# Optimization experiments

Hardware: AMD Instinct MI355X
Metric: run time of the kernel (lower is better)

## Reference

```python
import jax, jax.numpy as jnp
import numpy as np

N = 50000
E = 1_600_000
IN_C = 128
OUT_C = 128


def _glorot(key, shape):
    fan_in, fan_out = shape[0], shape[1]
    s = jnp.sqrt(6.0 / (fan_in + fan_out))
    return jax.random.uniform(key, shape, jnp.float32, -s, s)


def setup_inputs() -> dict:
    key = jax.random.key(0)
    ks = jax.random.split(key, 32)
    inp = {
        'X': jax.random.normal(ks[0], (N, IN_C), jnp.float32),
        'edge_index': jax.random.randint(ks[1], (2, E), 0, N, jnp.int64),
        'edge_weight': jax.random.uniform(ks[2], (E,), jnp.float32),
        'H': jax.random.normal(ks[3], (N, OUT_C), jnp.float32),
        'C': jax.random.normal(ks[4], (N, OUT_C), jnp.float32),
    }
    i = 5
    for g in ('i', 'f', 'c', 'o'):
        inp[f'Wx_{g}'] = _glorot(ks[i], (IN_C, OUT_C)); i += 1
        inp[f'bx_{g}'] = jnp.zeros((OUT_C,), jnp.float32)
        inp[f'Wh_{g}'] = _glorot(ks[i], (OUT_C, OUT_C)); i += 1
        inp[f'bh_{g}'] = jnp.zeros((OUT_C,), jnp.float32)
    for g in ('i', 'f', 'o'):
        inp[f'w_c_{g}'] = _glorot(ks[i], (1, OUT_C)); i += 1
    for g in ('i', 'f', 'c', 'o'):
        inp[f'b_{g}'] = jnp.zeros((1, OUT_C), jnp.float32)
    return inp


def reference(X, edge_index, edge_weight, H, C,
              Wx_i, bx_i, Wh_i, bh_i,
              Wx_f, bx_f, Wh_f, bh_f,
              Wx_c, bx_c, Wh_c, bh_c,
              Wx_o, bx_o, Wh_o, bh_o,
              w_c_i, w_c_f, w_c_o,
              b_i, b_f, b_c, b_o):
    n = X.shape[0]
    src, dst = edge_index[0], edge_index[1]
    # GCN normalization (add_self_loops=False): deg from destination (in-degree)
    deg = jax.ops.segment_sum(edge_weight, dst, num_segments=n)
    dis = jnp.where(deg > 0, jax.lax.rsqrt(jnp.where(deg > 0, deg, 1.0)), 0.0)
    norm = dis[src] * edge_weight * dis[dst]  # [E]

    def gcn(x, W, b):
        xw = x @ W                       # [n, OUT_C]
        msg = xw[src] * norm[:, None]    # gather + scale, [E, OUT_C]
        return jax.ops.segment_sum(msg, dst, num_segments=n) + b

    I = jax.nn.sigmoid(gcn(X, Wx_i, bx_i) + gcn(H, Wh_i, bh_i) + w_c_i * C + b_i)
    Fg = jax.nn.sigmoid(gcn(X, Wx_f, bx_f) + gcn(H, Wh_f, bh_f) + w_c_f * C + b_f)
    T = jnp.tanh(gcn(X, Wx_c, bx_c) + gcn(H, Wh_c, bh_c) + b_c)
    Cn = Fg * C + I * T
    O = jax.nn.sigmoid(gcn(X, Wx_o, bx_o) + gcn(H, Wh_o, bh_o) + w_c_o * Cn + b_o)
    Hn = O * jnp.tanh(Cn)
    return Hn, Cn
```

## Files before the change

### kernel.cpp

```cpp
#include <hip/hip_runtime.h>

__device__ __forceinline__ float bf2f(unsigned short u){
    union { unsigned int i; float f; } v; v.i = ((unsigned int)u) << 16; return v.f;
}
__device__ __forceinline__ unsigned short f2bf(float f){
    union { unsigned int i; float f; } v; v.f = f;
    unsigned int i = v.i;
    unsigned int r = i + 0x7FFFu + ((i >> 16) & 1u);
    return (unsigned short)(r >> 16);
}
__device__ __forceinline__ float sigm(float x){ return 1.0f / (1.0f + __expf(-x)); }

__device__ __forceinline__ float ldsel(const void* p, size_t idx, int fF){
    float r;
    if (fF) r = ((const float*)p)[idx];
    else    r = bf2f(((const unsigned short*)p)[idx]);
    return r;
}

typedef __attribute__((ext_vector_type(8))) short s8v;
typedef __attribute__((ext_vector_type(4))) float f4v;

__global__ void k_detect(const unsigned short* __restrict__ X,
                         const int* __restrict__ ei, int* __restrict__ flags){
    __shared__ int cnt, nz;
    if (threadIdx.x == 0){ cnt = 0; nz = 0; }
    __syncthreads();
    int ok = 0;
    for (int i = threadIdx.x; i < 2048; i += 256){
        int e = (X[i] >> 7) & 0xFF;
        if (e >= 96 && e <= 160) ok++;
    }
    atomicAdd(&cnt, ok);
    int nzl = 0;
    for (int i = threadIdx.x; i < 128; i += 256)
        if (ei[2*i + 1] != 0) nzl++;
    atomicAdd(&nz, nzl);
    __syncthreads();
    if (threadIdx.x == 0){
        flags[0] = (cnt < 1843) ? 1 : 0;
        flags[1] = (nz == 0)   ? 1 : 0;
    }
}

struct PackArgs {
    const void* Wx[4];
    const void* Wh[4];
    const void* bx[4];
    const void* bh[4];
};

__global__ void k_fused1(const void* __restrict__ X, const void* __restrict__ H,
                         unsigned int* __restrict__ XHb32,
                         const int* __restrict__ ei, int* __restrict__ cnt,
                         int* __restrict__ off,
                         PackArgs pa, unsigned short* __restrict__ Bp,
                         float* __restrict__ bias,
                         const int* __restrict__ flags,
                         int nbT, int nbC, int E, int N){
    int b = blockIdx.x;
    int fF = flags[0];
    if (b < nbT){
        int t = b*256 + threadIdx.x;
        if (t >= N * 64) return;
        int n = t >> 6, l = t & 63;
        unsigned int xw, hw;
        if (fF){
            float2 xv = ((const float2*)X)[(size_t)n*64 + l];
            float2 hv = ((const float2*)H)[(size_t)n*64 + l];
            xw = ((unsigned int)f2bf(xv.y) << 16) | f2bf(xv.x);
            hw = ((unsigned int)f2bf(hv.y) << 16) | f2bf(hv.x);
        } else {
            xw = ((const unsigned int*)X)[(size_t)n*64 + l];
            hw = ((const unsigned int*)H)[(size_t)n*64 + l];
        }
        XHb32[(size_t)n*128 + l]      = xw;
        XHb32[(size_t)n*128 + 64 + l] = hw;
    } else if (b < nbT + nbC){
        int e = (b - nbT)*256 + threadIdx.x;
        if (e >= E) return;
        int fI = flags[1];
        int d = fI ? ei[2*(size_t)E + 2*(size_t)e] : ei[(size_t)E + e];
        if ((unsigned)d >= (unsigned)N) return;
        off[e] = atomicAdd(&cnt[d], 1);
    } else {
        int t = (b - nbT - nbC)*256 + threadIdx.x;
        if (t < 4*8*8*64*8){
            int j    =  t        & 7;
            int lane = (t >> 3)  & 63;
            int kb   = (t >> 9)  & 7;
            int ct   = (t >> 12) & 7;
            int g    = (t >> 15) & 3;
            int k   = kb*32 + (lane >> 4)*8 + j;
            int col = ct*16 + (lane & 15);
            const void* p; size_t idx;
            if (k < 128){ p = pa.Wx[g]; idx = (size_t)k*128 + col; }
            else        { p = pa.Wh[g]; idx = (size_t)(k-128)*128 + col; }
            unsigned short v;
            if (fF) v = f2bf(((const float*)p)[idx]);
            else    v = ((const unsigned short*)p)[idx];
            Bp[t] = v;
        }
        if (t < 512){
            int g = t >> 7, c = t & 127;
            bias[t] = ldsel(pa.bx[g], c, fF) + ldsel(pa.bh[g], c, fF);
        }
    }
}

__global__ void k_scanA(const int* __restrict__ cnt, int* __restrict__ bsum, int n){
    __shared__ int sh[256];
    int t = threadIdx.x, i = blockIdx.x * 256 + t;
    sh[t] = (i < n) ? cnt[i] : 0;
    __syncthreads();
    for (int o = 128; o > 0; o >>= 1){
        if (t < o) sh[t] += sh[t + o];
        __syncthreads();
    }
    if (t == 0) bsum[blockIdx.x] = sh[0];
}
__global__ void k_scanB(const int* __restrict__ bsum, int* __restrict__ bsumoff, int nb){
    __shared__ int sh[256];
    int t = threadIdx.x;
    int v = (t < nb) ? bsum[t] : 0;
    sh[t] = v;
    __syncthreads();
    for (int o = 1; o < 256; o <<= 1){
        int u = (t >= o) ? sh[t - o] : 0;
        __syncthreads();
        sh[t] += u;
        __syncthreads();
    }
    bsumoff[t] = sh[t] - v;
}
__global__ void k_scanC(const int* __restrict__ cnt, const int* __restrict__ bsumoff,
                        int* __restrict__ rowstart, int n){
    __shared__ int sh[256];
    int t = threadIdx.x, i = blockIdx.x * 256 + t;
    int v = (i < n) ? cnt[i] : 0;
    sh[t] = v;
    __syncthreads();
    for (int o = 1; o < 256; o <<= 1){
        int u = (t >= o) ? sh[t - o] : 0;
        __syncthreads();
        sh[t] += u;
        __syncthreads();
    }
    int incl = sh[t];
    if (i < n)     rowstart[i] = bsumoff[blockIdx.x] + incl - v;
    if (i == n-1)  rowstart[n] = bsumoff[blockIdx.x] + incl;
}

__global__ void k_scatter(const int* __restrict__ ei, const void* __restrict__ ew,
                          const int* __restrict__ rowstart, const int* __restrict__ off,
                          int2* __restrict__ recs, const int* __restrict__ flags,
                          int E, int N){
    int e = blockIdx.x * 256 + threadIdx.x;
    if (e >= E) return;
    int fF = flags[0], fI = flags[1];
    int s, d;
    if (fI){ s = ei[2*(size_t)e]; d = ei[2*(size_t)E + 2*(size_t)e]; }
    else   { s = ei[e];           d = ei[(size_t)E + e]; }
    if ((unsigned)d >= (unsigned)N) return;
    float w = 0.f; int ss = 0;
    if ((unsigned)s < (unsigned)N){ w = ldsel(ew, e, fF); ss = s; }
    int2 r; r.x = ss; r.y = __float_as_int(w);
    recs[rowstart[d] + off[e]] = r;
}

__global__ __launch_bounds__(256)
void k_degdis(const int2* __restrict__ recs, const int* __restrict__ rowstart,
              float* __restrict__ dis, int N){
    int gw = (blockIdx.x * 256 + threadIdx.x) >> 6;
    int lane = threadIdx.x & 63;
    if (gw >= N) return;
    int beg = rowstart[gw], end = rowstart[gw + 1];
    float sw = 0.f;
    for (int i = beg + lane; i < end; i += 64) sw += __int_as_float(recs[i].y);
    for (int o = 32; o > 0; o >>= 1) sw += __shfl_down(sw, o);
    if (lane == 0) dis[gw] = (sw > 0.f) ? rsqrtf(sw) : 0.f;
}

__global__ __launch_bounds__(256)
void k_gather(const int2* __restrict__ recs, const int* __restrict__ rowstart,
              const float* __restrict__ dis, const unsigned int* __restrict__ XHb32,
              unsigned int* __restrict__ AXH32, int N){
    int gw = (blockIdx.x * 256 + threadIdx.x) >> 6;
    int lane = threadIdx.x & 63;
    if (gw >= 2*N) return;
    int node = gw >> 1;
    int half = (gw & 1) * 64;
    int beg = rowstart[node], end = rowstart[node + 1];
    float disd = dis[node];
    float a0 = 0.f, a1 = 0.f;
    int i = beg;
    for (; i + 1 < end; i += 2){
        int2 r1 = recs[i];
        int2 r2 = recs[i+1];
        float n1 = dis[r1.x] * __int_as_float(r1.y) * disd;
        float n2 = dis[r2.x] * __int_as_float(r2.y) * disd;
        unsigned int v1 = XHb32[(size_t)r1.x*128 + half + lane];
        unsigned int v2 = XHb32[(size_t)r2.x*128 + half + lane];
        a0 += n1 * bf2f((unsigned short)(v1 & 0xffff));
        a1 += n1 * bf2f((unsigned short)(v1 >> 16));
        a0 += n2 * bf2f((unsigned short)(v2 & 0xffff));
        a1 += n2 * bf2f((unsigned short)(v2 >> 16));
    }
    if (i < end){
        int2 r1 = recs[i];
        float n1 = dis[r1.x] * __int_as_float(r1.y) * disd;
        unsigned int v1 = XHb32[(size_t)r1.x*128 + half + lane];
        a0 += n1 * bf2f((unsigned short)(v1 & 0xffff));
        a1 += n1 * bf2f((unsigned short)(v1 >> 16));
    }
    AXH32[(size_t)node*128 + half + lane] = ((unsigned int)f2bf(a1) << 16) | f2bf(a0);
}

struct EpiArgs {
    const void *C, *wci, *wcf, *wco, *bi, *bff, *bc, *bo;
};

__global__ __launch_bounds__(256)
void k_gemm(const unsigned short* __restrict__ AXH,
            const unsigned short* __restrict__ Bp, const float* __restrict__ bias,
            EpiArgs ea, void* __restrict__ outp, const int* __restrict__ flags, int N){
    __shared__ float pre[4][16][132];

    int tid  = threadIdx.x;
    int wave = tid >> 6, lane = tid & 63;
    int node0 = blockIdx.x * 16;
    int fF = flags[0];

    f4v acc[8];
#pragma unroll
    for (int ct = 0; ct < 8; ct++) acc[ct] = (f4v){0.f,0.f,0.f,0.f};

    const int g = wave;
    const unsigned short* abase = AXH + (size_t)(node0 + (lane & 15))*256 + (lane >> 4)*8;
#pragma unroll
    for (int kb = 0; kb < 8; kb++){
        s8v af = *(const s8v*)(abase + kb*32);
        const unsigned short* bbase = Bp + g*32768 + kb*512 + lane*8;
#pragma unroll
        for (int ct = 0; ct < 8; ct++){
            s8v bfrag = *(const s8v*)(bbase + ct*4096);
            acc[ct] = __builtin_amdgcn_mfma_f32_16x16x32_bf16(af, bfrag, acc[ct], 0, 0, 0);
        }
    }

    int q = lane >> 4, cl = lane & 15;
#pragma unroll
    for (int ct = 0; ct < 8; ct++){
        int col = ct*16 + cl;
        float bv = bias[g*128 + col];
#pragma unroll
        for (int r = 0; r < 4; r++)
            pre[g][q*4 + r][col] = acc[ct][r] + bv;
    }
    __syncthreads();

    for (int i = tid; i < 2048; i += 256){
        int nn = i >> 7, c = i & 127;
        if (node0 + nn >= N) break;
        size_t gidx = (size_t)(node0+nn)*128 + c;
        float Cv  = ldsel(ea.C, gidx, fF);
        float pi  = pre[0][nn][c], pf = pre[1][nn][c];
        float pcv = pre[2][nn][c], po = pre[3][nn][c];
        float Iv = sigm(pi + ldsel(ea.wci, c, fF)*Cv + ldsel(ea.bi, c, fF));
        float Fv = sigm(pf + ldsel(ea.wcf, c, fF)*Cv + ldsel(ea.bff, c, fF));
        float Tv = tanhf(pcv + ldsel(ea.bc, c, fF));
        float Cn = Fv*Cv + Iv*Tv;
        float Ov = sigm(po + ldsel(ea.wco, c, fF)*Cn + ldsel(ea.bo, c, fF));
        float Hn = Ov * tanhf(Cn);
        if (fF){
            ((float*)outp)[gidx] = Hn;
            ((float*)outp)[(size_t)N*128 + gidx] = Cn;
        } else {
            ((unsigned short*)outp)[gidx] = f2bf(Hn);
            ((unsigned short*)outp)[(size_t)N*128 + gidx] = f2bf(Cn);
        }
    }
}

extern "C" void kernel_launch(void* const* d_in, const int* in_sizes, int n_in,
                              void* d_out, int out_size, void* d_ws, size_t ws_size,
                              hipStream_t stream){
    const void* X  = d_in[0];
    const int*  ei = (const int*)d_in[1];
    const void* ew = d_in[2];
    const void* H  = d_in[3];
    const void* C  = d_in[4];
    const int N = in_sizes[0] / 128;
    const int E = in_sizes[2];

    char* ws = (char*)d_ws;
    int*   cnt          = (int*)  (ws);
    float* dis          = (float*)(ws + ((size_t)256 << 10));
    int*   rowstart     = (int*)  (ws + ((size_t)512 << 10));
    int*   bsum         = (int*)  (ws + ((size_t)768 << 10));
    int*   bsumoff      = (int*)  (ws + ((size_t)772 << 10));
    int*   flags        = (int*)  (ws + ((size_t)776 << 10));
    unsigned short* Bp  = (unsigned short*)(ws + ((size_t)1 << 20));
    float* bias         = (float*)(ws + ((size_t)1 << 20) + ((size_t)256 << 10));
    int*   off          = (int*)  (ws + ((size_t)2 << 20));
    unsigned int* AXH32 = (unsigned int*)(ws + ((size_t)2 << 20));
    int2*  recs         = (int2*) (ws + ((size_t)28 << 20));
    unsigned int* XHb32 = (unsigned int*)(ws + ((size_t)41 << 20));

    hipMemsetAsync(cnt, 0, (size_t)256 << 10, stream);
    k_detect<<<1, 256, 0, stream>>>((const unsigned short*)X, ei, flags);

    PackArgs pa;
    pa.Wx[0]=d_in[5];  pa.bx[0]=d_in[6];  pa.Wh[0]=d_in[7];  pa.bh[0]=d_in[8];
    pa.Wx[1]=d_in[9];  pa.bx[1]=d_in[10]; pa.Wh[1]=d_in[11]; pa.bh[1]=d_in[12];
    pa.Wx[2]=d_in[13]; pa.bx[2]=d_in[14]; pa.Wh[2]=d_in[15]; pa.bh[2]=d_in[16];
    pa.Wx[3]=d_in[17]; pa.bx[3]=d_in[18]; pa.Wh[3]=d_in[19]; pa.bh[3]=d_in[20];

    int nbT = (N*64 + 255)/256;
    int nbC = (E + 255)/256;
    k_fused1<<<nbT + nbC + 512, 256, 0, stream>>>(X, H, XHb32, ei, cnt, off,
                                                  pa, Bp, bias, flags, nbT, nbC, E, N);

    int nbA = (N + 255)/256;
    k_scanA<<<nbA, 256, 0, stream>>>(cnt, bsum, N);
    k_scanB<<<1, 256, 0, stream>>>(bsum, bsumoff, nbA);
    k_scanC<<<nbA, 256, 0, stream>>>(cnt, bsumoff, rowstart, N);

    k_scatter<<<(E + 255)/256, 256, 0, stream>>>(ei, ew, rowstart, off, recs, flags, E, N);
    k_degdis<<<(N*64 + 255)/256, 256, 0, stream>>>(recs, rowstart, dis, N);
    k_gather<<<(2*N*64 + 255)/256, 256, 0, stream>>>(recs, rowstart, dis, XHb32, AXH32, N);

    EpiArgs ea;
    ea.C   = C;
    ea.wci = d_in[21];
    ea.wcf = d_in[22];
    ea.wco = d_in[23];
    ea.bi  = d_in[24];
    ea.bff = d_in[25];
    ea.bc  = d_in[26];
    ea.bo  = d_in[27];
    k_gemm<<<(N + 15)/16, 256, 0, stream>>>((const unsigned short*)AXH32, Bp, bias,
                                            ea, d_out, flags, N);
}
```

Before: 589.2 us.

## Fold degree into count pass, merge scans, precompute edge norms, widen GEMM tiles

Degree is now accumulated by float atomics in the edge-count pass, which removes the separate k_degdis kernel. dis is computed inside the scanA launch. The three-kernel scan becomes two by having each block sum the preceding block totals itself. Scatter stores the full normalized edge weight, so the gather no longer does random dis lookups and is unrolled by four. The GEMM processes 32 nodes per block, reusing each B fragment for two MFMAs. Risks: float atomics make degree summation order nondeterministic, and the per-block prefix sum reads is redundant work.

```diff
diff --git a/kernel.cpp b/kernel.cpp
--- a/kernel.cpp
+++ b/kernel.cpp
@@ -52,7 +52,8 @@
 
 __global__ void k_fused1(const void* __restrict__ X, const void* __restrict__ H,
                          unsigned int* __restrict__ XHb32,
-                         const int* __restrict__ ei, int* __restrict__ cnt,
+                         const int* __restrict__ ei, const void* __restrict__ ew,
+                         int* __restrict__ cnt, float* __restrict__ deg,
                          int* __restrict__ off,
                          PackArgs pa, unsigned short* __restrict__ Bp,
                          float* __restrict__ bias,
@@ -83,6 +84,7 @@
         int d = fI ? ei[2*(size_t)E + 2*(size_t)e] : ei[(size_t)E + e];
         if ((unsigned)d >= (unsigned)N) return;
         off[e] = atomicAdd(&cnt[d], 1);
+        atomicAdd(&deg[d], ldsel(ew, e, fF));
     } else {
         int t = (b - nbT - nbC)*256 + threadIdx.x;
         if (t < 4*8*8*64*8){
@@ -108,35 +110,39 @@
     }
 }
 
-__global__ void k_scanA(const int* __restrict__ cnt, int* __restrict__ bsum, int n){
-    __shared__ int sh[256];
-    int t = threadIdx.x, i = blockIdx.x * 256 + t;
-    sh[t] = (i < n) ? cnt[i] : 0;
-    __syncthreads();
-    for (int o = 128; o > 0; o >>= 1){
-        if (t < o) sh[t] += sh[t + o];
-        __syncthreads();
-    }
-    if (t == 0) bsum[blockIdx.x] = sh[0];
-}
-__global__ void k_scanB(const int* __restrict__ bsum, int* __restrict__ bsumoff, int nb){
-    __shared__ int sh[256];
-    int t = threadIdx.x;
-    int v = (t < nb) ? bsum[t] : 0;
-    sh[t] = v;
-    __syncthreads();
-    for (int o = 1; o < 256; o <<= 1){
-        int u = (t >= o) ? sh[t - o] : 0;
-        __syncthreads();
-        sh[t] += u;
-        __syncthreads();
-    }
-    bsumoff[t] = sh[t] - v;
-}
-__global__ void k_scanC(const int* __restrict__ cnt, const int* __restrict__ bsumoff,
+__global__ void k_scanA(const int* __restrict__ cnt, int* __restrict__ bsum,
+                        const float* __restrict__ deg, float* __restrict__ dis,
+                        int n, int nbA){
+    if ((int)blockIdx.x < nbA){
+        __shared__ int sh[256];
+        int t = threadIdx.x, i = blockIdx.x * 256 + t;
+        sh[t] = (i < n) ? cnt[i] : 0;
+        __syncthreads();
+        for (int o = 128; o > 0; o >>= 1){
+            if (t < o) sh[t] += sh[t + o];
+            __syncthreads();
+        }
+        if (t == 0) bsum[blockIdx.x] = sh[0];
+    } else {
+        int i = (blockIdx.x - nbA) * 256 + threadIdx.x;
+        if (i < n){ float d = deg[i]; dis[i] = (d > 0.f) ? rsqrtf(d) : 0.f; }
+    }
+}
+
+__global__ void k_scan2(const int* __restrict__ cnt, const int* __restrict__ bsum,
                         int* __restrict__ rowstart, int n){
     __shared__ int sh[256];
     int t = threadIdx.x, i = blockIdx.x * 256 + t;
+    int base = 0;
+    for (int j = t; j < (int)blockIdx.x; j += 256) base += bsum[j];
+    sh[t] = base;
+    __syncthreads();
+    for (int o = 128; o > 0; o >>= 1){
+        if (t < o) sh[t] += sh[t + o];
+        __syncthreads();
+    }
+    int blockoff = sh[0];
+    __syncthreads();
     int v = (i < n) ? cnt[i] : 0;
     sh[t] = v;
     __syncthreads();
@@ -147,11 +153,12 @@
         __syncthreads();
     }
     int incl = sh[t];
-    if (i < n)     rowstart[i] = bsumoff[blockIdx.x] + incl - v;
-    if (i == n-1)  rowstart[n] = bsumoff[blockIdx.x] + incl;
+    if (i < n)     rowstart[i] = blockoff + incl - v;
+    if (i == n-1)  rowstart[n] = blockoff + incl;
 }
 
 __global__ void k_scatter(const int* __restrict__ ei, const void* __restrict__ ew,
+                          const float* __restrict__ dis,
                           const int* __restrict__ rowstart, const int* __restrict__ off,
                           int2* __restrict__ recs, const int* __restrict__ flags,
                           int E, int N){
@@ -164,26 +171,14 @@
     if ((unsigned)d >= (unsigned)N) return;
     float w = 0.f; int ss = 0;
     if ((unsigned)s < (unsigned)N){ w = ldsel(ew, e, fF); ss = s; }
-    int2 r; r.x = ss; r.y = __float_as_int(w);
+    float nrm = dis[ss] * w * dis[d];
+    int2 r; r.x = ss; r.y = __float_as_int(nrm);
     recs[rowstart[d] + off[e]] = r;
-}
-
-__global__ __launch_bounds__(256)
-void k_degdis(const int2* __restrict__ recs, const int* __restrict__ rowstart,
-              float* __restrict__ dis, int N){
-    int gw = (blockIdx.x * 256 + threadIdx.x) >> 6;
-    int lane = threadIdx.x & 63;
-    if (gw >= N) return;
-    int beg = rowstart[gw], end = rowstart[gw + 1];
-    float sw = 0.f;
-    for (int i = beg + lane; i < end; i += 64) sw += __int_as_float(recs[i].y);
-    for (int o = 32; o > 0; o >>= 1) sw += __shfl_down(sw, o);
-    if (lane == 0) dis[gw] = (sw > 0.f) ? rsqrtf(sw) : 0.f;
 }
 
 __global__ __launch_bounds__(256)
 void k_gather(const int2* __restrict__ recs, const int* __restrict__ rowstart,
-              const float* __restrict__ dis, const unsigned int* __restrict__ XHb32,
+              const unsigned int* __restrict__ XHb32,
               unsigned int* __restrict__ AXH32, int N){
     int gw = (blockIdx.x * 256 + threadIdx.x) >> 6;
     int lane = threadIdx.x & 63;
@@ -191,27 +186,31 @@
     int node = gw >> 1;
     int half = (gw & 1) * 64;
     int beg = rowstart[node], end = rowstart[node + 1];
-    float disd = dis[node];
     float a0 = 0.f, a1 = 0.f;
     int i = beg;
-    for (; i + 1 < end; i += 2){
-        int2 r1 = recs[i];
-        int2 r2 = recs[i+1];
-        float n1 = dis[r1.x] * __int_as_float(r1.y) * disd;
-        float n2 = dis[r2.x] * __int_as_float(r2.y) * disd;
+    for (; i + 3 < end; i += 4){
+        int2 r0 = recs[i], r1 = recs[i+1], r2 = recs[i+2], r3 = recs[i+3];
+        unsigned int v0 = XHb32[(size_t)r0.x*128 + half + lane];
         unsigned int v1 = XHb32[(size_t)r1.x*128 + half + lane];
         unsigned int v2 = XHb32[(size_t)r2.x*128 + half + lane];
+        unsigned int v3 = XHb32[(size_t)r3.x*128 + half + lane];
+        float n0 = __int_as_float(r0.y), n1 = __int_as_float(r1.y);
+        float n2 = __int_as_float(r2.y), n3 = __int_as_float(r3.y);
+        a0 += n0 * bf2f((unsigned short)(v0 & 0xffff));
+        a1 += n0 * bf2f((unsigned short)(v0 >> 16));
         a0 += n1 * bf2f((unsigned short)(v1 & 0xffff));
         a1 += n1 * bf2f((unsigned short)(v1 >> 16));
         a0 += n2 * bf2f((unsigned short)(v2 & 0xffff));
         a1 += n2 * bf2f((unsigned short)(v2 >> 16));
-    }
-    if (i < end){
-        int2 r1 = recs[i];
-        float n1 = dis[r1.x] * __int_as_float(r1.y) * disd;
-        unsigned int v1 = XHb32[(size_t)r1.x*128 + half + lane];
-        a0 += n1 * bf2f((unsigned short)(v1 & 0xffff));
-        a1 += n1 * bf2f((unsigned short)(v1 >> 16));
+        a0 += n3 * bf2f((unsigned short)(v3 & 0xffff));
+        a1 += n3 * bf2f((unsigned short)(v3 >> 16));
+    }
+    for (; i < end; i++){
+        int2 r0 = recs[i];
+        float n0 = __int_as_float(r0.y);
+        unsigned int v0 = XHb32[(size_t)r0.x*128 + half + lane];
+        a0 += n0 * bf2f((unsigned short)(v0 & 0xffff));
+        a1 += n0 * bf2f((unsigned short)(v0 >> 16));
     }
     AXH32[(size_t)node*128 + half + lane] = ((unsigned int)f2bf(a1) << 16) | f2bf(a0);
 }
@@ -228,57 +227,66 @@
 
     int tid  = threadIdx.x;
     int wave = tid >> 6, lane = tid & 63;
-    int node0 = blockIdx.x * 16;
+    int node0 = blockIdx.x * 32;
     int fF = flags[0];
 
-    f4v acc[8];
-#pragma unroll
-    for (int ct = 0; ct < 8; ct++) acc[ct] = (f4v){0.f,0.f,0.f,0.f};
+    f4v acc[2][8];
+#pragma unroll
+    for (int m = 0; m < 2; m++)
+#pragma unroll
+        for (int ct = 0; ct < 8; ct++) acc[m][ct] = (f4v){0.f,0.f,0.f,0.f};
 
     const int g = wave;
-    const unsigned short* abase = AXH + (size_t)(node0 + (lane & 15))*256 + (lane >> 4)*8;
+    const unsigned short* abase0 = AXH + (size_t)(node0      + (lane & 15))*256 + (lane >> 4)*8;
+    const unsigned short* abase1 = AXH + (size_t)(node0 + 16 + (lane & 15))*256 + (lane >> 4)*8;
 #pragma unroll
     for (int kb = 0; kb < 8; kb++){
-        s8v af = *(const s8v*)(abase + kb*32);
+        s8v af0 = *(const s8v*)(abase0 + kb*32);
+        s8v af1 = *(const s8v*)(abase1 + kb*32);
         const unsigned short* bbase = Bp + g*32768 + kb*512 + lane*8;
 #pragma unroll
         for (int ct = 0; ct < 8; ct++){
             s8v bfrag = *(const s8v*)(bbase + ct*4096);
-            acc[ct] = __builtin_amdgcn_mfma_f32_16x16x32_bf16(af, bfrag, acc[ct], 0, 0, 0);
+            acc[0][ct] = __builtin_amdgcn_mfma_f32_16x16x32_bf16(af0, bfrag, acc[0][ct], 0, 0, 0);
+            acc[1][ct] = __builtin_amdgcn_mfma_f32_16x16x32_bf16(af1, bfrag, acc[1][ct], 0, 0, 0);
         }
     }
 
     int q = lane >> 4, cl = lane & 15;
-#pragma unroll
-    for (int ct = 0; ct < 8; ct++){
-        int col = ct*16 + cl;
-        float bv = bias[g*128 + col];
-#pragma unroll
-        for (int r = 0; r < 4; r++)
-            pre[g][q*4 + r][col] = acc[ct][r] + bv;
-    }
-    __syncthreads();
-
-    for (int i = tid; i < 2048; i += 256){
-        int nn = i >> 7, c = i & 127;
-        if (node0 + nn >= N) break;
-        size_t gidx = (size_t)(node0+nn)*128 + c;
-        float Cv  = ldsel(ea.C, gidx, fF);
-        float pi  = pre[0][nn][c], pf = pre[1][nn][c];
-        float pcv = pre[2][nn][c], po = pre[3][nn][c];
-        float Iv = sigm(pi + ldsel(ea.wci, c, fF)*Cv + ldsel(ea.bi, c, fF));
-        float Fv = sigm(pf + ldsel(ea.wcf, c, fF)*Cv + ldsel(ea.bff, c, fF));
-        float Tv = tanhf(pcv + ldsel(ea.bc, c, fF));
-        float Cn = Fv*Cv + Iv*Tv;
-        float Ov = sigm(po + ldsel(ea.wco, c, fF)*Cn + ldsel(ea.bo, c, fF));
-        float Hn = Ov * tanhf(Cn);
-        if (fF){
-            ((float*)outp)[gidx] = Hn;
-            ((float*)outp)[(size_t)N*128 + gidx] = Cn;
-        } else {
-            ((unsigned short*)outp)[gidx] = f2bf(Hn);
-            ((unsigned short*)outp)[(size_t)N*128 + gidx] = f2bf(Cn);
-        }
+    for (int m = 0; m < 2; m++){
+        int nbase = node0 + m*16;
+#pragma unroll
+        for (int ct = 0; ct < 8; ct++){
+            int col = ct*16 + cl;
+            float bv = bias[g*128 + col];
+#pragma unroll
+            for (int r = 0; r < 4; r++)
+                pre[g][q*4 + r][col] = acc[m][ct][r] + bv;
+        }
+        __syncthreads();
+
+        for (int i = tid; i < 2048; i += 256){
+            int nn = i >> 7, c = i & 127;
+            if (nbase + nn >= N) break;
+            size_t gidx = (size_t)(nbase+nn)*128 + c;
+            float Cv  = ldsel(ea.C, gidx, fF);
+            float pi  = pre[0][nn][c], pf = pre[1][nn][c];
+            float pcv = pre[2][nn][c], po = pre[3][nn][c];
+            float Iv = sigm(pi + ldsel(ea.wci, c, fF)*Cv + ldsel(ea.bi, c, fF));
+            float Fv = sigm(pf + ldsel(ea.wcf, c, fF)*Cv + ldsel(ea.bff, c, fF));
+            float Tv = tanhf(pcv + ldsel(ea.bc, c, fF));
+            float Cn = Fv*Cv + Iv*Tv;
+            float Ov = sigm(po + ldsel(ea.wco, c, fF)*Cn + ldsel(ea.bo, c, fF));
+            float Hn = Ov * tanhf(Cn);
+            if (fF){
+                ((float*)outp)[gidx] = Hn;
+                ((float*)outp)[(size_t)N*128 + gidx] = Cn;
+            } else {
+                ((unsigned short*)outp)[gidx] = f2bf(Hn);
+                ((unsigned short*)outp)[(size_t)N*128 + gidx] = f2bf(Cn);
+            }
+        }
+        __syncthreads();
     }
 }
 
@@ -295,19 +303,19 @@
 
     char* ws = (char*)d_ws;
     int*   cnt          = (int*)  (ws);
-    float* dis          = (float*)(ws + ((size_t)256 << 10));
-    int*   rowstart     = (int*)  (ws + ((size_t)512 << 10));
-    int*   bsum         = (int*)  (ws + ((size_t)768 << 10));
-    int*   bsumoff      = (int*)  (ws + ((size_t)772 << 10));
-    int*   flags        = (int*)  (ws + ((size_t)776 << 10));
-    unsigned short* Bp  = (unsigned short*)(ws + ((size_t)1 << 20));
-    float* bias         = (float*)(ws + ((size_t)1 << 20) + ((size_t)256 << 10));
+    float* deg          = (float*)(ws + ((size_t)256 << 10));
+    float* dis          = (float*)(ws + ((size_t)512 << 10));
+    int*   rowstart     = (int*)  (ws + ((size_t)768 << 10));
+    int*   bsum         = (int*)  (ws + ((size_t)1028 << 10));
+    int*   flags        = (int*)  (ws + ((size_t)1032 << 10));
+    unsigned short* Bp  = (unsigned short*)(ws + ((size_t)1280 << 10));
+    float* bias         = (float*)(ws + ((size_t)1536 << 10));
     int*   off          = (int*)  (ws + ((size_t)2 << 20));
     unsigned int* AXH32 = (unsigned int*)(ws + ((size_t)2 << 20));
     int2*  recs         = (int2*) (ws + ((size_t)28 << 20));
     unsigned int* XHb32 = (unsigned int*)(ws + ((size_t)41 << 20));
 
-    hipMemsetAsync(cnt, 0, (size_t)256 << 10, stream);
+    hipMemsetAsync(ws, 0, (size_t)512 << 10, stream);
     k_detect<<<1, 256, 0, stream>>>((const unsigned short*)X, ei, flags);
 
     PackArgs pa;
@@ -318,17 +326,16 @@
 
     int nbT = (N*64 + 255)/256;
     int nbC = (E + 255)/256;
-    k_fused1<<<nbT + nbC + 512, 256, 0, stream>>>(X, H, XHb32, ei, cnt, off,
+    k_fused1<<<nbT + nbC + 512, 256, 0, stream>>>(X, H, XHb32, ei, ew, cnt, deg, off,
                                                   pa, Bp, bias, flags, nbT, nbC, E, N);
 
     int nbA = (N + 255)/256;
-    k_scanA<<<nbA, 256, 0, stream>>>(cnt, bsum, N);
-    k_scanB<<<1, 256, 0, stream>>>(bsum, bsumoff, nbA);
-    k_scanC<<<nbA, 256, 0, stream>>>(cnt, bsumoff, rowstart, N);
-
-    k_scatter<<<(E + 255)/256, 256, 0, stream>>>(ei, ew, rowstart, off, recs, flags, E, N);
-    k_degdis<<<(N*64 + 255)/256, 256, 0, stream>>>(recs, rowstart, dis, N);
-    k_gather<<<(2*N*64 + 255)/256, 256, 0, stream>>>(recs, rowstart, dis, XHb32, AXH32, N);
+    k_scanA<<<nbA + nbA, 256, 0, stream>>>(cnt, bsum, deg, dis, N, nbA);
+    k_scan2<<<nbA, 256, 0, stream>>>(cnt, bsum, rowstart, N);
+
+    k_scatter<<<(E + 255)/256, 256, 0, stream>>>(ei, ew, dis, rowstart, off,
+                                                 recs, flags, E, N);
+    k_gather<<<(2*N*64 + 255)/256, 256, 0, stream>>>(recs, rowstart, XHb32, AXH32, N);
 
     EpiArgs ea;
     ea.C   = C;
@@ -339,6 +346,6 @@
     ea.bff = d_in[25];
     ea.bc  = d_in[26];
     ea.bo  = d_in[27];
-    k_gemm<<<(N + 15)/16, 256, 0, stream>>>((const unsigned short*)AXH32, Bp, bias,
+    k_gemm<<<(N + 31)/32, 256, 0, stream>>>((const unsigned short*)AXH32, Bp, bias,
                                             ea, d_out, flags, N);
 }
```

After: 629.2 us. +6.8%, slower.
